# Performance work log

Hardware: AMD Instinct MI355X
Metric: run time of the kernel (lower is better)

## Reference

```python
import jax, jax.numpy as jnp
import numpy as np

N, E, FE = 20000, 160000, 500000
IN, HC, HEADS = 128, 64, 4
HEADC = HC // HEADS          # 16
DV = HEADC                   # 16
KHOP = 3
NUM_T = 128
OUT = 1
CST = 1e-5


def _lin(key, fan_in, fan_out):
    kw, kb = jax.random.split(key)
    s = 1.0 / np.sqrt(fan_in)
    W = jax.random.uniform(kw, (fan_in, fan_out), minval=-s, maxval=s, dtype=jnp.float32)
    b = jax.random.uniform(kb, (fan_out,), minval=-s, maxval=s, dtype=jnp.float32)
    return W, b


def setup_inputs() -> dict:
    key = jax.random.key(0)
    ks = jax.random.split(key, 16)
    x = jax.random.normal(ks[0], (N, IN), dtype=jnp.float32)
    edge_index = jax.random.randint(ks[1], (2, E), 0, N, dtype=jnp.int32)
    full_edge_index = jax.random.randint(ks[2], (2, FE), 0, N, dtype=jnp.int32)
    time_steps = jax.random.randint(ks[3], (N,), 0, NUM_T, dtype=jnp.int32)
    Wi, bi = _lin(ks[4], IN, HC)
    Wt1, bt1 = _lin(ks[5], HC, 4 * HC)
    Wt2, bt2 = _lin(ks[6], 4 * HC, HC)
    WQ, bQ = _lin(ks[7], HC, HEADS * HEADC)
    WK, bK = _lin(ks[8], HC, HEADS * HEADC)
    WV, bV = _lin(ks[9], HC, HEADS * DV)
    Wo, bo = _lin(ks[10], HEADS * DV, DV)
    hopwise = jnp.ones((KHOP + 1,), dtype=jnp.float32)
    headwise = jnp.zeros((HEADS, KHOP), dtype=jnp.float32)
    Wf1, bf1 = _lin(ks[11], 2 * DV, DV)
    Wf2, bf2 = _lin(ks[12], DV, OUT)
    return dict(x=x, edge_index=edge_index, full_edge_index=full_edge_index,
                time_steps=time_steps, Wi=Wi, bi=bi, Wt1=Wt1, bt1=bt1,
                Wt2=Wt2, bt2=bt2, WQ=WQ, bQ=bQ, WK=WK, bK=bK, WV=WV, bV=bV,
                Wo=Wo, bo=bo, hopwise=hopwise, headwise=headwise,
                Wf1=Wf1, bf1=bf1, Wf2=Wf2, bf2=bf2)


def _sin_emb(t, dim, num_steps, rescale=4000.0):
    # Sinusoidal timestep embedding rescaled by num_steps (diffusion style).
    t = t.astype(jnp.float32) * (rescale / num_steps)
    half = dim // 2
    freqs = jnp.exp(-jnp.log(10000.0) / (half - 1) * jnp.arange(half, dtype=jnp.float32))
    args = t[:, None] * freqs[None, :]
    return jnp.concatenate([jnp.sin(args), jnp.cos(args)], axis=-1)


def reference(x, edge_index, full_edge_index, time_steps,
              Wi, bi, Wt1, bt1, Wt2, bt2, WQ, bQ, WK, bK, WV, bV,
              Wo, bo, hopwise, headwise, Wf1, bf1, Wf2, bf2):
    n = x.shape[0]
    row, col = edge_index[0], edge_index[1]

    # random-walk norm: deg over destination (col), norm gathered at source (row)
    deg = jax.ops.segment_sum(jnp.ones_like(col, dtype=x.dtype), col, num_segments=n)
    deg_inv = jnp.where(deg > 0, 1.0 / deg, 0.0)
    norm = deg_inv[row]                                   # [E]

    t_emb = _sin_emb(time_steps, HC, NUM_T)               # [N, HC]
    t_emb = jax.nn.silu(t_emb @ Wt1 + bt1) @ Wt2 + bt2    # [N, HC]

    h = jax.nn.relu(x @ Wi + bi + t_emb)                  # [N, HC]

    Q = (1.0 + jax.nn.elu(h @ WQ + bQ)).reshape(n, HEADS, HEADC)
    Kf = (1.0 + jax.nn.elu(h @ WK + bK)).reshape(n, HEADS, HEADC)
    V = (h @ WV + bV).reshape(n, HEADS, DV)

    M = jnp.einsum('nhi,nhj->nhij', Kf, V)                # [N, H, hc, dv]
    hidden = V * hopwise[0]
    layerwise = jax.nn.softmax(headwise, axis=0)          # softmax over heads

    for hop in range(KHOP):
        # gather-scale-scatter message passing (random walk propagation)
        M = jax.ops.segment_sum(M[row] * norm[:, None, None, None], col, num_segments=n)
        Kf = jax.ops.segment_sum(Kf[row] * norm[:, None, None], col, num_segments=n)
        H = jnp.einsum('nhi,nhij->nhj', Q, M)             # [N, H, dv]
        C = jnp.einsum('nhi,nhi->nh', Q, Kf)[..., None] + CST
        gamma = hopwise[hop + 1] * layerwise[:, hop][:, None]   # [H, 1]
        hidden = hidden + gamma * (H / C)

    # multi_concat output projection
    hidden = hidden.reshape(n, HEADS * DV) @ Wo + bo      # [N, DV]

    src, dst = full_edge_index[0], full_edge_index[1]
    he = jnp.concatenate([hidden[src], hidden[dst]], axis=-1)  # [FE, 2*DV]
    edge_logits = jax.nn.silu(he @ Wf1 + bf1) @ Wf2 + bf2      # [FE, OUT]
    return edge_logits, hidden
```

## Files before the change

kernel.cpp:

```cpp
#include <hip/hip_runtime.h>
#include <math.h>


#define HC 64
#define HEADS 4
#define KHOP 3
#define NUM_T 128
#define MSZ 1024
#define SLOTS 64
#define CST 1e-5f

typedef float f32x2 __attribute__((ext_vector_type(2)));

__device__ __forceinline__ float bf2f(unsigned short s) { return __uint_as_float(((unsigned int)s) << 16); }
__device__ __forceinline__ float bfu_lo(unsigned int u) { return __uint_as_float(u << 16); }
__device__ __forceinline__ float bfu_hi(unsigned int u) { return __uint_as_float(u & 0xffff0000u); }
__device__ __forceinline__ unsigned short f2bf(float f) {
    unsigned int u = __float_as_uint(f);
    u = (u + 0x7fffu + ((u >> 16) & 1u)) >> 16;
    return (unsigned short)u;
}
__device__ __forceinline__ unsigned int pack4fp8(float a, float b, float c, float d) {
    int r = __builtin_amdgcn_cvt_pk_fp8_f32(a, b, 0, false);
    r = __builtin_amdgcn_cvt_pk_fp8_f32(c, d, r, true);
    return (unsigned int)r;
}

__global__ __launch_bounds__(256) void k_pre(
    const int* __restrict__ row, const int* __restrict__ col,
    int* __restrict__ cnt, int* __restrict__ csr, int E, int fillBlocks,
    const float* __restrict__ Wt1, const float* __restrict__ bt1,
    const float* __restrict__ Wt2, const float* __restrict__ bt2,
    const float* __restrict__ hopwise, const float* __restrict__ headwise,
    float* __restrict__ gamma, float* __restrict__ table) {
    int b = blockIdx.x;
    if (b < fillBlocks) {
        int e = b * 256 + threadIdx.x;
        if (e < E) {
            int c = col[e];
            int r = row[e];
            int k = atomicAdd(&cnt[c], 1);
            if (k < SLOTS) csr[c * SLOTS + k] = r;
        }
        return;
    }
    int tval = b - fillBlocks;
    int t = threadIdx.x;
    if (tval == 0 && t == 0) {
        for (int k = 0; k < KHOP; k++) {
            float m = -1e30f;
            for (int h2 = 0; h2 < HEADS; h2++) m = fmaxf(m, headwise[h2 * KHOP + k]);
            float ex[HEADS]; float s = 0.f;
            for (int h2 = 0; h2 < HEADS; h2++) { ex[h2] = expf(headwise[h2 * KHOP + k] - m); s += ex[h2]; }
            for (int h2 = 0; h2 < HEADS; h2++) gamma[k * HEADS + h2] = hopwise[k + 1] * ex[h2] / s;
        }
    }
    __shared__ float emb_s[64];
    __shared__ float z1_s[256];
    __shared__ float ps_s[4][64];
    if (t < 64) {
        float tt = (float)tval * 31.25f;
        float e;
        if (t < 32) e = sinf(tt * expf(-0.2971077539347156f * (float)t));
        else        e = cosf(tt * expf(-0.2971077539347156f * (float)(t - 32)));
        emb_s[t] = e;
    }
    __syncthreads();
    {
        float acc = bt1[t];
        #pragma unroll 8
        for (int i = 0; i < 64; i++) acc += emb_s[i] * Wt1[i * 256 + t];
        z1_s[t] = acc / (1.f + expf(-acc));
    }
    __syncthreads();
    {
        int j = t & 63, p = t >> 6;
        float acc = 0.f;
        #pragma unroll 8
        for (int i = 0; i < 64; i++) acc += z1_s[p * 64 + i] * Wt2[(p * 64 + i) * 64 + j];
        ps_s[p][j] = acc;
    }
    __syncthreads();
    if (t < 64)
        table[tval * 64 + t] = ps_s[0][t] + ps_s[1][t] + ps_s[2][t] + ps_s[3][t] + bt2[t];
}

__global__ __launch_bounds__(256) void k_node(
    const float* __restrict__ x, const int* __restrict__ time_steps,
    const float* __restrict__ temb, const float* __restrict__ Wi,
    const float* __restrict__ bi,
    const float* __restrict__ WQ, const float* __restrict__ bQ,
    const float* __restrict__ WK, const float* __restrict__ bK,
    const float* __restrict__ WV, const float* __restrict__ bV,
    const float* __restrict__ hopwise, const int* __restrict__ cnt,
    float* __restrict__ Q, unsigned short* __restrict__ Kf0,
    unsigned short* __restrict__ Vbuf, float* __restrict__ hidden, int n) {
    __shared__ float xs[16][128];
    __shared__ float hs[16][64];
    int j = threadIdx.x & 63;
    int slot = threadIdx.x >> 6;
    int nbase = blockIdx.x * 16;
    int nvalid = min(16, n - nbase);
    const float4* xg = (const float4*)(x + (size_t)nbase * 128);
    float4* xs4 = (float4*)&xs[0][0];
    for (int idx = threadIdx.x; idx < nvalid * 32; idx += 256) xs4[idx] = xg[idx];
    __syncthreads();
    int nl = slot * 4;
    {
        float acc[4];
        #pragma unroll
        for (int k = 0; k < 4; k++) acc[k] = 0.f;
        #pragma unroll 8
        for (int i = 0; i < 128; i++) {
            float w = Wi[i * 64 + j];
            #pragma unroll
            for (int k = 0; k < 4; k++) acc[k] += xs[nl + k][i] * w;
        }
        float bj = bi[j];
        #pragma unroll
        for (int k = 0; k < 4; k++) {
            int node = nbase + nl + k;
            float te = (node < n) ? temb[time_steps[node] * 64 + j] : 0.f;
            hs[nl + k][j] = fmaxf(acc[k] + bj + te, 0.f);
        }
    }
    __syncthreads();
    float aq[4], ak[4], av[4];
    #pragma unroll
    for (int k = 0; k < 4; k++) { aq[k] = bQ[j]; ak[k] = bK[j]; av[k] = bV[j]; }
    #pragma unroll 4
    for (int i = 0; i < 64; i++) {
        float wq = WQ[i * 64 + j], wk = WK[i * 64 + j], wv = WV[i * 64 + j];
        #pragma unroll
        for (int k = 0; k < 4; k++) {
            float hv = hs[nl + k][i];
            aq[k] += hv * wq; ak[k] += hv * wk; av[k] += hv * wv;
        }
    }
    float h0 = hopwise[0];
    #pragma unroll
    for (int k = 0; k < 4; k++) {
        int node = nbase + nl + k;
        if (node < n) {
            float q  = 1.f + ((aq[k] > 0.f) ? aq[k] : (expf(aq[k]) - 1.f));
            float kf = 1.f + ((ak[k] > 0.f) ? ak[k] : (expf(ak[k]) - 1.f));
            int dg = min(cnt[node], SLOTS);
            float inv = (dg > 0) ? 1.0f / (float)dg : 0.0f;
            Q[(size_t)node * 64 + j] = q;
            Kf0[(size_t)node * 64 + j] = f2bf(kf * inv);
            Vbuf[(size_t)node * 64 + j] = f2bf(av[k]);
            hidden[(size_t)node * 64 + j] = av[k] * h0;
        }
    }
}

template<int MODE>
__global__ __launch_bounds__(128) void k_hop(
    const unsigned char* __restrict__ Mold, const unsigned short* __restrict__ Kfold,
    const unsigned short* __restrict__ Vbuf,
    const int* __restrict__ cnt, const int* __restrict__ csr,
    const float* __restrict__ Q, const float* __restrict__ gamma,
    unsigned char* __restrict__ Mnew, unsigned short* __restrict__ Kfnew,
    float* __restrict__ hidden, int hop, int write_out,
    const float* __restrict__ Wo, const float* __restrict__ bo,
    const float* __restrict__ Wf1, float* __restrict__ out16,
    float* __restrict__ Pbuf, int n) {
    constexpr int DEPTH = (MODE == 0) ? 4 : 8;
    int lane = threadIdx.x & 63;
    int node = blockIdx.x * 2 + (threadIdx.x >> 6);
    if (node >= n) return;
    int grp = lane >> 4;
    int deg = min(cnt[node], SLOTS);
    int sidx = __builtin_nontemporal_load(csr + (size_t)node * SLOTS + lane);
    float qv = Q[(size_t)node * 64 + lane];
    size_t hoff = (size_t)node * 64 + lane;
    float hid_in = hidden[hoff];
    int degU = __builtin_amdgcn_readfirstlane(deg);
    float acc[16];
    #pragma unroll
    for (int t = 0; t < 16; t++) acc[t] = 0.f;
    float kacc = 0.f;

    int d = 0;
    for (; d + DEPTH <= degU; d += DEPTH) {
        unsigned short kraw[DEPTH];
        uint4 m0[DEPTH], m1[DEPTH];
        #pragma unroll
        for (int t = 0; t < DEPTH; t++) {
            int s = __builtin_amdgcn_readlane(sidx, d + t);
            kraw[t] = Kfold[(size_t)s * 64 + lane];
            if constexpr (MODE == 0) {
                const uint4* vp = (const uint4*)((const unsigned char*)Vbuf + (size_t)s * 128 + grp * 32);
                m0[t] = vp[0]; m1[t] = vp[1];
            } else {
                m0[t] = *(const uint4*)(Mold + (size_t)s * MSZ + lane * 16);
            }
        }
        #pragma unroll
        for (int t = 0; t < DEPTH; t++) {
            float kf = bf2f(kraw[t]);
            kacc += kf;
            if constexpr (MODE == 0) {
                acc[0]  = fmaf(kf, bfu_lo(m0[t].x), acc[0]);
                acc[1]  = fmaf(kf, bfu_hi(m0[t].x), acc[1]);
                acc[2]  = fmaf(kf, bfu_lo(m0[t].y), acc[2]);
                acc[3]  = fmaf(kf, bfu_hi(m0[t].y), acc[3]);
                acc[4]  = fmaf(kf, bfu_lo(m0[t].z), acc[4]);
                acc[5]  = fmaf(kf, bfu_hi(m0[t].z), acc[5]);
                acc[6]  = fmaf(kf, bfu_lo(m0[t].w), acc[6]);
                acc[7]  = fmaf(kf, bfu_hi(m0[t].w), acc[7]);
                acc[8]  = fmaf(kf, bfu_lo(m1[t].x), acc[8]);
                acc[9]  = fmaf(kf, bfu_hi(m1[t].x), acc[9]);
                acc[10] = fmaf(kf, bfu_lo(m1[t].y), acc[10]);
                acc[11] = fmaf(kf, bfu_hi(m1[t].y), acc[11]);
                acc[12] = fmaf(kf, bfu_lo(m1[t].z), acc[12]);
                acc[13] = fmaf(kf, bfu_hi(m1[t].z), acc[13]);
                acc[14] = fmaf(kf, bfu_lo(m1[t].w), acc[14]);
                acc[15] = fmaf(kf, bfu_hi(m1[t].w), acc[15]);
            } else {
                f32x2 p;
                p = __builtin_amdgcn_cvt_pk_f32_fp8((int)m0[t].x, false); acc[0]  += p.x; acc[1]  += p.y;
                p = __builtin_amdgcn_cvt_pk_f32_fp8((int)m0[t].x, true);  acc[2]  += p.x; acc[3]  += p.y;
                p = __builtin_amdgcn_cvt_pk_f32_fp8((int)m0[t].y, false); acc[4]  += p.x; acc[5]  += p.y;
                p = __builtin_amdgcn_cvt_pk_f32_fp8((int)m0[t].y, true);  acc[6]  += p.x; acc[7]  += p.y;
                p = __builtin_amdgcn_cvt_pk_f32_fp8((int)m0[t].z, false); acc[8]  += p.x; acc[9]  += p.y;
                p = __builtin_amdgcn_cvt_pk_f32_fp8((int)m0[t].z, true);  acc[10] += p.x; acc[11] += p.y;
                p = __builtin_amdgcn_cvt_pk_f32_fp8((int)m0[t].w, false); acc[12] += p.x; acc[13] += p.y;
                p = __builtin_amdgcn_cvt_pk_f32_fp8((int)m0[t].w, true);  acc[14] += p.x; acc[15] += p.y;
            }
        }
    }
    if (d < degU) {
        int rem = degU - d;
        unsigned short kraw[DEPTH];
        uint4 m0[DEPTH], m1[DEPTH];
        #pragma unroll
        for (int t = 0; t < DEPTH - 1; t++) {
            if (t < rem) {
                int s = __builtin_amdgcn_readlane(sidx, d + t);
                kraw[t] = Kfold[(size_t)s * 64 + lane];
                if constexpr (MODE == 0) {
                    const uint4* vp = (const uint4*)((const unsigned char*)Vbuf + (size_t)s * 128 + grp * 32);
                    m0[t] = vp[0]; m1[t] = vp[1];
                } else {
                    m0[t] = *(const uint4*)(Mold + (size_t)s * MSZ + lane * 16);
                }
            }
        }
        #pragma unroll
        for (int t = 0; t < DEPTH - 1; t++) {
            if (t < rem) {
                float kf = bf2f(kraw[t]);
                kacc += kf;
                if constexpr (MODE == 0) {
                    acc[0]  = fmaf(kf, bfu_lo(m0[t].x), acc[0]);
                    acc[1]  = fmaf(kf, bfu_hi(m0[t].x), acc[1]);
                    acc[2]  = fmaf(kf, bfu_lo(m0[t].y), acc[2]);
                    acc[3]  = fmaf(kf, bfu_hi(m0[t].y), acc[3]);
                    acc[4]  = fmaf(kf, bfu_lo(m0[t].z), acc[4]);
                    acc[5]  = fmaf(kf, bfu_hi(m0[t].z), acc[5]);
                    acc[6]  = fmaf(kf, bfu_lo(m0[t].w), acc[6]);
                    acc[7]  = fmaf(kf, bfu_hi(m0[t].w), acc[7]);
                    acc[8]  = fmaf(kf, bfu_lo(m1[t].x), acc[8]);
                    acc[9]  = fmaf(kf, bfu_hi(m1[t].x), acc[9]);
                    acc[10] = fmaf(kf, bfu_lo(m1[t].y), acc[10]);
                    acc[11] = fmaf(kf, bfu_hi(m1[t].y), acc[11]);
                    acc[12] = fmaf(kf, bfu_lo(m1[t].z), acc[12]);
                    acc[13] = fmaf(kf, bfu_hi(m1[t].z), acc[13]);
                    acc[14] = fmaf(kf, bfu_lo(m1[t].w), acc[14]);
                    acc[15] = fmaf(kf, bfu_hi(m1[t].w), acc[15]);
                } else {
                    f32x2 p;
                    p = __builtin_amdgcn_cvt_pk_f32_fp8((int)m0[t].x, false); acc[0]  += p.x; acc[1]  += p.y;
                    p = __builtin_amdgcn_cvt_pk_f32_fp8((int)m0[t].x, true);  acc[2]  += p.x; acc[3]  += p.y;
                    p = __builtin_amdgcn_cvt_pk_f32_fp8((int)m0[t].y, false); acc[4]  += p.x; acc[5]  += p.y;
                    p = __builtin_amdgcn_cvt_pk_f32_fp8((int)m0[t].y, true);  acc[6]  += p.x; acc[7]  += p.y;
                    p = __builtin_amdgcn_cvt_pk_f32_fp8((int)m0[t].z, false); acc[8]  += p.x; acc[9]  += p.y;
                    p = __builtin_amdgcn_cvt_pk_f32_fp8((int)m0[t].z, true);  acc[10] += p.x; acc[11] += p.y;
                    p = __builtin_amdgcn_cvt_pk_f32_fp8((int)m0[t].w, false); acc[12] += p.x; acc[13] += p.y;
                    p = __builtin_amdgcn_cvt_pk_f32_fp8((int)m0[t].w, true);  acc[14] += p.x; acc[15] += p.y;
                }
            }
        }
    }

    if (write_out) {
        float inv = (degU > 0) ? 1.0f / (float)degU : 0.0f;
        uint4 st;
        st.x = pack4fp8(acc[0] * inv,  acc[1] * inv,  acc[2] * inv,  acc[3] * inv);
        st.y = pack4fp8(acc[4] * inv,  acc[5] * inv,  acc[6] * inv,  acc[7] * inv);
        st.z = pack4fp8(acc[8] * inv,  acc[9] * inv,  acc[10] * inv, acc[11] * inv);
        st.w = pack4fp8(acc[12] * inv, acc[13] * inv, acc[14] * inv, acc[15] * inv);
        *(uint4*)(Mnew + (size_t)node * MSZ + lane * 16) = st;
        Kfnew[(size_t)node * 64 + lane] = f2bf(kacc * inv);
    }

    float c = qv * kacc;
    c += __shfl_xor(c, 1); c += __shfl_xor(c, 2); c += __shfl_xor(c, 4); c += __shfl_xor(c, 8);

    float w0[16];
    #pragma unroll
    for (int t = 0; t < 16; t++) w0[t] = qv * acc[t];
    float w1r[8];
    #pragma unroll
    for (int t = 0; t < 8; t++) {
        float a = w0[2 * t], b = w0[2 * t + 1];
        float mine = (lane & 1) ? b : a, th = (lane & 1) ? a : b;
        w1r[t] = mine + __shfl_xor(th, 1);
    }
    float w2r[4];
    #pragma unroll
    for (int t = 0; t < 4; t++) {
        float a = w1r[2 * t], b = w1r[2 * t + 1];
        float mine = (lane & 2) ? b : a, th = (lane & 2) ? a : b;
        w2r[t] = mine + __shfl_xor(th, 2);
    }
    float w3r[2];
    #pragma unroll
    for (int t = 0; t < 2; t++) {
        float a = w2r[2 * t], b = w2r[2 * t + 1];
        float mine = (lane & 4) ? b : a, th = (lane & 4) ? a : b;
        w3r[t] = mine + __shfl_xor(th, 4);
    }
    float Hv;
    {
        float a = w3r[0], b = w3r[1];
        float mine = (lane & 8) ? b : a, th = (lane & 8) ? a : b;
        Hv = mine + __shfl_xor(th, 8);
    }

    float g = gamma[hop * HEADS + grp];
    float contrib = g * Hv / (c + CST);
    if (write_out) {
        hidden[hoff] = hid_in + contrib;
    } else {
        float hid = hid_in + contrib;
        const float4* wop = (const float4*)(Wo + lane * 16);
        float4 wo0 = wop[0], wo1 = wop[1], wo2 = wop[2], wo3 = wop[3];
        float v[16];
        v[0] = hid * wo0.x;  v[1] = hid * wo0.y;  v[2] = hid * wo0.z;  v[3] = hid * wo0.w;
        v[4] = hid * wo1.x;  v[5] = hid * wo1.y;  v[6] = hid * wo1.z;  v[7] = hid * wo1.w;
        v[8] = hid * wo2.x;  v[9] = hid * wo2.y;  v[10] = hid * wo2.z; v[11] = hid * wo2.w;
        v[12] = hid * wo3.x; v[13] = hid * wo3.y; v[14] = hid * wo3.z; v[15] = hid * wo3.w;
        #pragma unroll
        for (int m = 32; m >= 1; m >>= 1) {
            #pragma unroll
            for (int o = 0; o < 16; o++) v[o] += __shfl_xor(v[o], m);
        }
        #pragma unroll
        for (int o = 0; o < 16; o++) v[o] += bo[o];
        if (lane == 0) {
            float4* op = (float4*)(out16 + (size_t)node * 16);
            op[0] = make_float4(v[0],  v[1],  v[2],  v[3]);
            op[1] = make_float4(v[4],  v[5],  v[6],  v[7]);
            op[2] = make_float4(v[8],  v[9],  v[10], v[11]);
            op[3] = make_float4(v[12], v[13], v[14], v[15]);
        }
        if (lane < 32) {
            int o = lane & 15, half = lane >> 4;
            const float* wf = Wf1 + (size_t)(half * 16) * 16 + o;
            float p = 0.f;
            #pragma unroll
            for (int i = 0; i < 16; i++) p += v[i] * wf[i * 16];
            Pbuf[(size_t)node * 32 + lane] = p;
        }
    }
}

__global__ __launch_bounds__(256) void k_edge(
    const int* __restrict__ src, const int* __restrict__ dst,
    const float* __restrict__ Pbuf,
    const float* __restrict__ bf1, const float* __restrict__ Wf2,
    const float* __restrict__ bf2,
    float* __restrict__ out, int fe) {
    __shared__ float b1[16];
    __shared__ float w2[16];
    __shared__ float b2s;
    int t = threadIdx.x;
    if (t < 16) { b1[t] = bf1[t]; w2[t] = Wf2[t]; }
    if (t == 0) b2s = bf2[0];
    __syncthreads();
    int e = blockIdx.x * 256 + t;
    if (e >= fe) return;
    int s = src[e], d = dst[e];
    const float4* p1 = (const float4*)(Pbuf + (size_t)s * 32);
    const float4* p2 = (const float4*)(Pbuf + (size_t)d * 32 + 16);
    float z[16];
    #pragma unroll
    for (int q = 0; q < 4; q++) {
        float4 a = p1[q]; float4 b = p2[q];
        z[q * 4 + 0] = a.x + b.x; z[q * 4 + 1] = a.y + b.y;
        z[q * 4 + 2] = a.z + b.z; z[q * 4 + 3] = a.w + b.w;
    }
    float acc = b2s;
    #pragma unroll
    for (int o = 0; o < 16; o++) {
        float zz = z[o] + b1[o];
        zz = zz / (1.f + expf(-zz));
        acc += zz * w2[o];
    }
    out[e] = acc;
}

extern "C" void kernel_launch(void* const* d_in, const int* in_sizes, int n_in,
                              void* d_out, int out_size, void* d_ws, size_t ws_size,
                              hipStream_t stream) {
    const float* x        = (const float*)d_in[0];
    const int*   eidx     = (const int*)d_in[1];
    const int*   feidx    = (const int*)d_in[2];
    const int*   tsteps   = (const int*)d_in[3];
    const float* Wi  = (const float*)d_in[4];
    const float* bi  = (const float*)d_in[5];
    const float* Wt1 = (const float*)d_in[6];
    const float* bt1 = (const float*)d_in[7];
    const float* Wt2 = (const float*)d_in[8];
    const float* bt2 = (const float*)d_in[9];
    const float* WQ  = (const float*)d_in[10];
    const float* bQ  = (const float*)d_in[11];
    const float* WK  = (const float*)d_in[12];
    const float* bK  = (const float*)d_in[13];
    const float* WV  = (const float*)d_in[14];
    const float* bV  = (const float*)d_in[15];
    const float* Wo  = (const float*)d_in[16];
    const float* bo  = (const float*)d_in[17];
    const float* hopwise  = (const float*)d_in[18];
    const float* headwise = (const float*)d_in[19];
    const float* Wf1 = (const float*)d_in[20];
    const float* bf1 = (const float*)d_in[21];
    const float* Wf2 = (const float*)d_in[22];
    const float* bf2 = (const float*)d_in[23];

    const int N  = in_sizes[3];
    const int E  = in_sizes[1] / 2;
    const int FE = in_sizes[2] / 2;
    const int* row = eidx;
    const int* col = eidx + E;
    const int* fsrc = feidx;
    const int* fdst = feidx + FE;

    char* ws = (char*)d_ws;
    size_t off = 0;
    auto alloc = [&](size_t bytes) -> char* {
        char* p = ws + off;
        off = (off + bytes + 255) & ~(size_t)255;
        return p;
    };
    float* gamma     = (float*)alloc(KHOP * HEADS * sizeof(float));
    int*   cnt       = (int*)alloc((size_t)N * 4);
    int*   csr       = (int*)alloc((size_t)N * SLOTS * 4);
    float* temb      = (float*)alloc((size_t)NUM_T * HC * 4);
    float* Qbuf      = (float*)alloc((size_t)N * HC * 4);
    unsigned short* Kf0  = (unsigned short*)alloc((size_t)N * HC * 2);
    unsigned short* Kf_a = (unsigned short*)alloc((size_t)N * HC * 2);
    unsigned short* Kf_b = (unsigned short*)alloc((size_t)N * HC * 2);
    unsigned short* Vbuf = (unsigned short*)alloc((size_t)N * HC * 2);
    float* hidden    = (float*)alloc((size_t)N * HC * 4);
    unsigned char* M_a = (unsigned char*)alloc((size_t)N * MSZ);
    unsigned char* M_b = (unsigned char*)alloc((size_t)N * MSZ);
    float* Pbuf      = (float*)alloc((size_t)N * 32 * 4);
    (void)ws_size;

    float* out_edges = (float*)d_out;
    float* out_hid16 = (float*)d_out + FE;

    const int fillBlocks = (E + 255) / 256;
    const int preBlocks  = fillBlocks + NUM_T;
    const int hopBlocks  = (N + 1) / 2;

    (void)hipMemsetAsync(cnt, 0, (size_t)N * 4, stream);
    k_pre<<<preBlocks, 256, 0, stream>>>(row, col, cnt, csr, E, fillBlocks,
                                         Wt1, bt1, Wt2, bt2, hopwise, headwise,
                                         gamma, temb);
    k_node<<<(N + 15) / 16, 256, 0, stream>>>(x, tsteps, temb, Wi, bi,
                                              WQ, bQ, WK, bK, WV, bV, hopwise, cnt,
                                              Qbuf, Kf0, Vbuf, hidden, N);
    k_hop<0><<<hopBlocks, 128, 0, stream>>>(nullptr, Kf0, Vbuf, cnt, csr, Qbuf, gamma,
                                            M_a, Kf_a, hidden, 0, 1, Wo, bo, Wf1,
                                            out_hid16, Pbuf, N);
    k_hop<1><<<hopBlocks, 128, 0, stream>>>(M_a, Kf_a, nullptr, cnt, csr, Qbuf, gamma,
                                            M_b, Kf_b, hidden, 1, 1, Wo, bo, Wf1,
                                            out_hid16, Pbuf, N);
    k_hop<1><<<hopBlocks, 128, 0, stream>>>(M_b, Kf_b, nullptr, cnt, csr, Qbuf, gamma,
                                            M_a, Kf_a, hidden, 2, 0, Wo, bo, Wf1,
                                            out_hid16, Pbuf, N);
    k_edge<<<(FE + 255) / 256, 256, 0, stream>>>(fsrc, fdst, Pbuf, bf1, Wf2, bf2,
                                                 out_edges, FE);
}
```

Baseline: 259.2 us.

## Split hop kernel and remap dense FP8 hops to 128 threads per node

Hops 1 and 2 move from the templated k_hop (64 lanes per node, each loading 16 FP8 bytes per neighbour) to a new k_dense kernel. There, 128 threads per node each load 8 bytes per neighbour, read neighbour indices directly from the CSR, and reduce H/C and the output projection through shared memory instead of wave shuffles. Hop 0 becomes its own specialised kernel. The intent is more memory-level parallelism and lower register pressure for the gather of 1 KB M rows, at the cost of extra __syncthreads and serial per-thread dot products in the epilogue.

```diff
diff --git a/kernel.cpp b/kernel.cpp
--- a/kernel.cpp
+++ b/kernel.cpp
@@ -154,24 +154,19 @@
     }
 }
 
-template<int MODE>
-__global__ __launch_bounds__(128) void k_hop(
-    const unsigned char* __restrict__ Mold, const unsigned short* __restrict__ Kfold,
-    const unsigned short* __restrict__ Vbuf,
+__global__ __launch_bounds__(128) void k_hop0(
+    const unsigned short* __restrict__ Kfold, const unsigned short* __restrict__ Vbuf,
     const int* __restrict__ cnt, const int* __restrict__ csr,
     const float* __restrict__ Q, const float* __restrict__ gamma,
     unsigned char* __restrict__ Mnew, unsigned short* __restrict__ Kfnew,
-    float* __restrict__ hidden, int hop, int write_out,
-    const float* __restrict__ Wo, const float* __restrict__ bo,
-    const float* __restrict__ Wf1, float* __restrict__ out16,
-    float* __restrict__ Pbuf, int n) {
-    constexpr int DEPTH = (MODE == 0) ? 4 : 8;
+    float* __restrict__ hidden, int n) {
+    constexpr int DEPTH = 4;
     int lane = threadIdx.x & 63;
     int node = blockIdx.x * 2 + (threadIdx.x >> 6);
     if (node >= n) return;
     int grp = lane >> 4;
     int deg = min(cnt[node], SLOTS);
-    int sidx = __builtin_nontemporal_load(csr + (size_t)node * SLOTS + lane);
+    int sidx = csr[(size_t)node * SLOTS + lane];
     float qv = Q[(size_t)node * 64 + lane];
     size_t hoff = (size_t)node * 64 + lane;
     float hid_in = hidden[hoff];
@@ -189,18 +184,49 @@
         for (int t = 0; t < DEPTH; t++) {
             int s = __builtin_amdgcn_readlane(sidx, d + t);
             kraw[t] = Kfold[(size_t)s * 64 + lane];
-            if constexpr (MODE == 0) {
-                const uint4* vp = (const uint4*)((const unsigned char*)Vbuf + (size_t)s * 128 + grp * 32);
-                m0[t] = vp[0]; m1[t] = vp[1];
-            } else {
-                m0[t] = *(const uint4*)(Mold + (size_t)s * MSZ + lane * 16);
-            }
+            const uint4* vp = (const uint4*)((const unsigned char*)Vbuf + (size_t)s * 128 + grp * 32);
+            m0[t] = vp[0]; m1[t] = vp[1];
         }
         #pragma unroll
         for (int t = 0; t < DEPTH; t++) {
             float kf = bf2f(kraw[t]);
             kacc += kf;
-            if constexpr (MODE == 0) {
+            acc[0]  = fmaf(kf, bfu_lo(m0[t].x), acc[0]);
+            acc[1]  = fmaf(kf, bfu_hi(m0[t].x), acc[1]);
+            acc[2]  = fmaf(kf, bfu_lo(m0[t].y), acc[2]);
+            acc[3]  = fmaf(kf, bfu_hi(m0[t].y), acc[3]);
+            acc[4]  = fmaf(kf, bfu_lo(m0[t].z), acc[4]);
+            acc[5]  = fmaf(kf, bfu_hi(m0[t].z), acc[5]);
+            acc[6]  = fmaf(kf, bfu_lo(m0[t].w), acc[6]);
+            acc[7]  = fmaf(kf, bfu_hi(m0[t].w), acc[7]);
+            acc[8]  = fmaf(kf, bfu_lo(m1[t].x), acc[8]);
+            acc[9]  = fmaf(kf, bfu_hi(m1[t].x), acc[9]);
+            acc[10] = fmaf(kf, bfu_lo(m1[t].y), acc[10]);
+            acc[11] = fmaf(kf, bfu_hi(m1[t].y), acc[11]);
+            acc[12] = fmaf(kf, bfu_lo(m1[t].z), acc[12]);
+            acc[13] = fmaf(kf, bfu_hi(m1[t].z), acc[13]);
+            acc[14] = fmaf(kf, bfu_lo(m1[t].w), acc[14]);
+            acc[15] = fmaf(kf, bfu_hi(m1[t].w), acc[15]);
+        }
+    }
+    if (d < degU) {
+        int rem = degU - d;
+        unsigned short kraw[DEPTH];
+        uint4 m0[DEPTH], m1[DEPTH];
+        #pragma unroll
+        for (int t = 0; t < DEPTH - 1; t++) {
+            if (t < rem) {
+                int s = __builtin_amdgcn_readlane(sidx, d + t);
+                kraw[t] = Kfold[(size_t)s * 64 + lane];
+                const uint4* vp = (const uint4*)((const unsigned char*)Vbuf + (size_t)s * 128 + grp * 32);
+                m0[t] = vp[0]; m1[t] = vp[1];
+            }
+        }
+        #pragma unroll
+        for (int t = 0; t < DEPTH - 1; t++) {
+            if (t < rem) {
+                float kf = bf2f(kraw[t]);
+                kacc += kf;
                 acc[0]  = fmaf(kf, bfu_lo(m0[t].x), acc[0]);
                 acc[1]  = fmaf(kf, bfu_hi(m0[t].x), acc[1]);
                 acc[2]  = fmaf(kf, bfu_lo(m0[t].y), acc[2]);
@@ -217,74 +243,11 @@
                 acc[13] = fmaf(kf, bfu_hi(m1[t].z), acc[13]);
                 acc[14] = fmaf(kf, bfu_lo(m1[t].w), acc[14]);
                 acc[15] = fmaf(kf, bfu_hi(m1[t].w), acc[15]);
-            } else {
-                f32x2 p;
-                p = __builtin_amdgcn_cvt_pk_f32_fp8((int)m0[t].x, false); acc[0]  += p.x; acc[1]  += p.y;
-                p = __builtin_amdgcn_cvt_pk_f32_fp8((int)m0[t].x, true);  acc[2]  += p.x; acc[3]  += p.y;
-                p = __builtin_amdgcn_cvt_pk_f32_fp8((int)m0[t].y, false); acc[4]  += p.x; acc[5]  += p.y;
-                p = __builtin_amdgcn_cvt_pk_f32_fp8((int)m0[t].y, true);  acc[6]  += p.x; acc[7]  += p.y;
-                p = __builtin_amdgcn_cvt_pk_f32_fp8((int)m0[t].z, false); acc[8]  += p.x; acc[9]  += p.y;
-                p = __builtin_amdgcn_cvt_pk_f32_fp8((int)m0[t].z, true);  acc[10] += p.x; acc[11] += p.y;
-                p = __builtin_amdgcn_cvt_pk_f32_fp8((int)m0[t].w, false); acc[12] += p.x; acc[13] += p.y;
-                p = __builtin_amdgcn_cvt_pk_f32_fp8((int)m0[t].w, true);  acc[14] += p.x; acc[15] += p.y;
             }
         }
     }
-    if (d < degU) {
-        int rem = degU - d;
-        unsigned short kraw[DEPTH];
-        uint4 m0[DEPTH], m1[DEPTH];
-        #pragma unroll
-        for (int t = 0; t < DEPTH - 1; t++) {
-            if (t < rem) {
-                int s = __builtin_amdgcn_readlane(sidx, d + t);
-                kraw[t] = Kfold[(size_t)s * 64 + lane];
-                if constexpr (MODE == 0) {
-                    const uint4* vp = (const uint4*)((const unsigned char*)Vbuf + (size_t)s * 128 + grp * 32);
-                    m0[t] = vp[0]; m1[t] = vp[1];
-                } else {
-                    m0[t] = *(const uint4*)(Mold + (size_t)s * MSZ + lane * 16);
-                }
-            }
-        }
-        #pragma unroll
-        for (int t = 0; t < DEPTH - 1; t++) {
-            if (t < rem) {
-                float kf = bf2f(kraw[t]);
-                kacc += kf;
-                if constexpr (MODE == 0) {
-                    acc[0]  = fmaf(kf, bfu_lo(m0[t].x), acc[0]);
-                    acc[1]  = fmaf(kf, bfu_hi(m0[t].x), acc[1]);
-                    acc[2]  = fmaf(kf, bfu_lo(m0[t].y), acc[2]);
-                    acc[3]  = fmaf(kf, bfu_hi(m0[t].y), acc[3]);
-                    acc[4]  = fmaf(kf, bfu_lo(m0[t].z), acc[4]);
-                    acc[5]  = fmaf(kf, bfu_hi(m0[t].z), acc[5]);
-                    acc[6]  = fmaf(kf, bfu_lo(m0[t].w), acc[6]);
-                    acc[7]  = fmaf(kf, bfu_hi(m0[t].w), acc[7]);
-                    acc[8]  = fmaf(kf, bfu_lo(m1[t].x), acc[8]);
-                    acc[9]  = fmaf(kf, bfu_hi(m1[t].x), acc[9]);
-                    acc[10] = fmaf(kf, bfu_lo(m1[t].y), acc[10]);
-                    acc[11] = fmaf(kf, bfu_hi(m1[t].y), acc[11]);
-                    acc[12] = fmaf(kf, bfu_lo(m1[t].z), acc[12]);
-                    acc[13] = fmaf(kf, bfu_hi(m1[t].z), acc[13]);
-                    acc[14] = fmaf(kf, bfu_lo(m1[t].w), acc[14]);
-                    acc[15] = fmaf(kf, bfu_hi(m1[t].w), acc[15]);
-                } else {
-                    f32x2 p;
-                    p = __builtin_amdgcn_cvt_pk_f32_fp8((int)m0[t].x, false); acc[0]  += p.x; acc[1]  += p.y;
-                    p = __builtin_amdgcn_cvt_pk_f32_fp8((int)m0[t].x, true);  acc[2]  += p.x; acc[3]  += p.y;
-                    p = __builtin_amdgcn_cvt_pk_f32_fp8((int)m0[t].y, false); acc[4]  += p.x; acc[5]  += p.y;
-                    p = __builtin_amdgcn_cvt_pk_f32_fp8((int)m0[t].y, true);  acc[6]  += p.x; acc[7]  += p.y;
-                    p = __builtin_amdgcn_cvt_pk_f32_fp8((int)m0[t].z, false); acc[8]  += p.x; acc[9]  += p.y;
-                    p = __builtin_amdgcn_cvt_pk_f32_fp8((int)m0[t].z, true);  acc[10] += p.x; acc[11] += p.y;
-                    p = __builtin_amdgcn_cvt_pk_f32_fp8((int)m0[t].w, false); acc[12] += p.x; acc[13] += p.y;
-                    p = __builtin_amdgcn_cvt_pk_f32_fp8((int)m0[t].w, true);  acc[14] += p.x; acc[15] += p.y;
-                }
-            }
-        }
-    }
-
-    if (write_out) {
+
+    {
         float inv = (degU > 0) ? 1.0f / (float)degU : 0.0f;
         uint4 st;
         st.x = pack4fp8(acc[0] * inv,  acc[1] * inv,  acc[2] * inv,  acc[3] * inv);
@@ -329,40 +292,116 @@
         Hv = mine + __shfl_xor(th, 8);
     }
 
-    float g = gamma[hop * HEADS + grp];
-    float contrib = g * Hv / (c + CST);
-    if (write_out) {
-        hidden[hoff] = hid_in + contrib;
-    } else {
-        float hid = hid_in + contrib;
-        const float4* wop = (const float4*)(Wo + lane * 16);
-        float4 wo0 = wop[0], wo1 = wop[1], wo2 = wop[2], wo3 = wop[3];
-        float v[16];
-        v[0] = hid * wo0.x;  v[1] = hid * wo0.y;  v[2] = hid * wo0.z;  v[3] = hid * wo0.w;
-        v[4] = hid * wo1.x;  v[5] = hid * wo1.y;  v[6] = hid * wo1.z;  v[7] = hid * wo1.w;
-        v[8] = hid * wo2.x;  v[9] = hid * wo2.y;  v[10] = hid * wo2.z; v[11] = hid * wo2.w;
-        v[12] = hid * wo3.x; v[13] = hid * wo3.y; v[14] = hid * wo3.z; v[15] = hid * wo3.w;
-        #pragma unroll
-        for (int m = 32; m >= 1; m >>= 1) {
+    float g = gamma[0 * HEADS + grp];
+    hidden[hoff] = hid_in + g * Hv / (c + CST);
+}
+
+__global__ __launch_bounds__(256) void k_dense(
+    const unsigned char* __restrict__ Mold, const unsigned short* __restrict__ Kfold,
+    const int* __restrict__ cnt, const int* __restrict__ csr,
+    const float* __restrict__ Q, const float* __restrict__ gamma,
+    unsigned char* __restrict__ Mnew, unsigned short* __restrict__ Kfnew,
+    float* __restrict__ hidden, int hop, int write_out,
+    const float* __restrict__ Wo, const float* __restrict__ bo,
+    const float* __restrict__ Wf1, float* __restrict__ out16,
+    float* __restrict__ Pbuf, int n) {
+    int group = threadIdx.x >> 7;
+    int gtid  = threadIdx.x & 127;
+    int node  = blockIdx.x * 2 + group;
+    int off   = gtid * 8;
+    __shared__ float sm[2][MSZ];
+    __shared__ float sk[2][64];
+    __shared__ float sh[2][64];
+    __shared__ float so[2][16];
+    bool valid = (node < n);
+    float acc[8];
+    #pragma unroll
+    for (int t = 0; t < 8; t++) acc[t] = 0.f;
+    float kacc = 0.f;
+    if (valid) {
+        int deg = min(cnt[node], SLOTS);
+        const int* lst = csr + (size_t)node * SLOTS;
+        int d = 0;
+        for (; d + 4 <= deg; d += 4) {
+            int s0 = lst[d + 0], s1 = lst[d + 1], s2 = lst[d + 2], s3 = lst[d + 3];
+            uint2 m0 = *(const uint2*)(Mold + (size_t)s0 * MSZ + off);
+            uint2 m1 = *(const uint2*)(Mold + (size_t)s1 * MSZ + off);
+            uint2 m2 = *(const uint2*)(Mold + (size_t)s2 * MSZ + off);
+            uint2 m3 = *(const uint2*)(Mold + (size_t)s3 * MSZ + off);
+            float kr0 = 0.f, kr1 = 0.f, kr2 = 0.f, kr3 = 0.f;
+            if (gtid < 64) {
+                kr0 = bf2f(Kfold[(size_t)s0 * 64 + gtid]);
+                kr1 = bf2f(Kfold[(size_t)s1 * 64 + gtid]);
+                kr2 = bf2f(Kfold[(size_t)s2 * 64 + gtid]);
+                kr3 = bf2f(Kfold[(size_t)s3 * 64 + gtid]);
+            }
+            const uint2 mm[4] = {m0, m1, m2, m3};
             #pragma unroll
-            for (int o = 0; o < 16; o++) v[o] += __shfl_xor(v[o], m);
-        }
-        #pragma unroll
-        for (int o = 0; o < 16; o++) v[o] += bo[o];
-        if (lane == 0) {
-            float4* op = (float4*)(out16 + (size_t)node * 16);
-            op[0] = make_float4(v[0],  v[1],  v[2],  v[3]);
-            op[1] = make_float4(v[4],  v[5],  v[6],  v[7]);
-            op[2] = make_float4(v[8],  v[9],  v[10], v[11]);
-            op[3] = make_float4(v[12], v[13], v[14], v[15]);
-        }
-        if (lane < 32) {
-            int o = lane & 15, half = lane >> 4;
+            for (int p = 0; p < 4; p++) {
+                f32x2 q;
+                q = __builtin_amdgcn_cvt_pk_f32_fp8((int)mm[p].x, false); acc[0] += q.x; acc[1] += q.y;
+                q = __builtin_amdgcn_cvt_pk_f32_fp8((int)mm[p].x, true);  acc[2] += q.x; acc[3] += q.y;
+                q = __builtin_amdgcn_cvt_pk_f32_fp8((int)mm[p].y, false); acc[4] += q.x; acc[5] += q.y;
+                q = __builtin_amdgcn_cvt_pk_f32_fp8((int)mm[p].y, true);  acc[6] += q.x; acc[7] += q.y;
+            }
+            if (gtid < 64) kacc += (kr0 + kr1) + (kr2 + kr3);
+        }
+        for (; d < deg; d++) {
+            int s = lst[d];
+            uint2 mv = *(const uint2*)(Mold + (size_t)s * MSZ + off);
+            f32x2 q;
+            q = __builtin_amdgcn_cvt_pk_f32_fp8((int)mv.x, false); acc[0] += q.x; acc[1] += q.y;
+            q = __builtin_amdgcn_cvt_pk_f32_fp8((int)mv.x, true);  acc[2] += q.x; acc[3] += q.y;
+            q = __builtin_amdgcn_cvt_pk_f32_fp8((int)mv.y, false); acc[4] += q.x; acc[5] += q.y;
+            q = __builtin_amdgcn_cvt_pk_f32_fp8((int)mv.y, true);  acc[6] += q.x; acc[7] += q.y;
+            if (gtid < 64) kacc += bf2f(Kfold[(size_t)s * 64 + gtid]);
+        }
+        float4* dst = (float4*)&sm[group][off];
+        dst[0] = make_float4(acc[0], acc[1], acc[2], acc[3]);
+        dst[1] = make_float4(acc[4], acc[5], acc[6], acc[7]);
+        if (gtid < 64) sk[group][gtid] = kacc;
+        if (write_out) {
+            float inv = (deg > 0) ? 1.0f / (float)deg : 0.0f;
+            uint2 st;
+            st.x = pack4fp8(acc[0] * inv, acc[1] * inv, acc[2] * inv, acc[3] * inv);
+            st.y = pack4fp8(acc[4] * inv, acc[5] * inv, acc[6] * inv, acc[7] * inv);
+            *(uint2*)(Mnew + (size_t)node * MSZ + off) = st;
+            if (gtid < 64) Kfnew[(size_t)node * 64 + gtid] = f2bf(kacc * inv);
+        }
+    }
+    __syncthreads();
+    if (valid && gtid < 64) {
+        int hh = gtid >> 4, j = gtid & 15;
+        const float* qn = Q + (size_t)node * 64 + hh * 16;
+        float C = CST, H = 0.f;
+        #pragma unroll
+        for (int i = 0; i < 16; i++) {
+            float qv = qn[i];
+            C += qv * sk[group][hh * 16 + i];
+            H += qv * sm[group][hh * 256 + i * 16 + j];
+        }
+        float g = gamma[hop * HEADS + hh];
+        float hid = hidden[(size_t)node * 64 + gtid] + g * H / C;
+        if (write_out) hidden[(size_t)node * 64 + gtid] = hid;
+        else sh[group][gtid] = hid;
+    }
+    if (!write_out) {
+        __syncthreads();
+        if (valid && gtid < 16) {
+            float a = bo[gtid];
+            #pragma unroll 8
+            for (int i = 0; i < 64; i++) a += sh[group][i] * Wo[i * 16 + gtid];
+            out16[(size_t)node * 16 + gtid] = a;
+            so[group][gtid] = a;
+        }
+        __syncthreads();
+        if (valid && gtid < 32) {
+            int o = gtid & 15, half = gtid >> 4;
             const float* wf = Wf1 + (size_t)(half * 16) * 16 + o;
             float p = 0.f;
             #pragma unroll
-            for (int i = 0; i < 16; i++) p += v[i] * wf[i * 16];
-            Pbuf[(size_t)node * 32 + lane] = p;
+            for (int i = 0; i < 16; i++) p += so[group][i] * wf[i * 16];
+            Pbuf[(size_t)node * 32 + gtid] = p;
         }
     }
 }
@@ -474,15 +513,14 @@
     k_node<<<(N + 15) / 16, 256, 0, stream>>>(x, tsteps, temb, Wi, bi,
                                               WQ, bQ, WK, bK, WV, bV, hopwise, cnt,
                                               Qbuf, Kf0, Vbuf, hidden, N);
-    k_hop<0><<<hopBlocks, 128, 0, stream>>>(nullptr, Kf0, Vbuf, cnt, csr, Qbuf, gamma,
-                                            M_a, Kf_a, hidden, 0, 1, Wo, bo, Wf1,
-                                            out_hid16, Pbuf, N);
-    k_hop<1><<<hopBlocks, 128, 0, stream>>>(M_a, Kf_a, nullptr, cnt, csr, Qbuf, gamma,
-                                            M_b, Kf_b, hidden, 1, 1, Wo, bo, Wf1,
-                                            out_hid16, Pbuf, N);
-    k_hop<1><<<hopBlocks, 128, 0, stream>>>(M_b, Kf_b, nullptr, cnt, csr, Qbuf, gamma,
-                                            M_a, Kf_a, hidden, 2, 0, Wo, bo, Wf1,
-                                            out_hid16, Pbuf, N);
+    k_hop0<<<hopBlocks, 128, 0, stream>>>(Kf0, Vbuf, cnt, csr, Qbuf, gamma,
+                                          M_a, Kf_a, hidden, N);
+    k_dense<<<hopBlocks, 256, 0, stream>>>(M_a, Kf_a, cnt, csr, Qbuf, gamma,
+                                           M_b, Kf_b, hidden, 1, 1, Wo, bo, Wf1,
+                                           out_hid16, Pbuf, N);
+    k_dense<<<hopBlocks, 256, 0, stream>>>(M_b, Kf_b, cnt, csr, Qbuf, gamma,
+                                           M_a, Kf_a, hidden, 2, 0, Wo, bo, Wf1,
+                                           out_hid16, Pbuf, N);
     k_edge<<<(FE + 255) / 256, 256, 0, stream>>>(fsrc, fdst, Pbuf, bf1, Wf2, bf2,
                                                  out_edges, FE);
 }
```

New measurement: 253.7 us (median of 2 runs). -2.1%, faster.
